# Kernel tuning notes

Measured on AMD Instinct MI355X. Metric: run time of the kernel, lower is better.

Reference implementation:

```python
import jax, jax.numpy as jnp
import numpy as np

NA, NP_, E = 40000, 60000, 80000
D, H = 512, 8
DK = D // H
SQRT_DK = float(DK) ** 0.5


def setup_inputs() -> dict:
    key = jax.random.key(0)
    ks = list(jax.random.split(key, 20))
    it = iter(ks)

    def nrm(shape, scale=1.0):
        return jax.random.normal(next(it), shape, dtype=jnp.float32) * scale

    xav = (6.0 / (DK + DK)) ** 0.5  # xavier_uniform bound for (dk, dk)
    w_scale = D ** -0.5
    inp = {
        "h_author": nrm((NA, D)),
        "h_paper": nrm((NP_, D)),
        "writes_src": jax.random.randint(next(it), (E,), 0, NA, dtype=jnp.int32),
        "writes_dst": jax.random.randint(next(it), (E,), 0, NP_, dtype=jnp.int32),
        "cites_src": jax.random.randint(next(it), (E,), 0, NP_, dtype=jnp.int32),
        "cites_dst": jax.random.randint(next(it), (E,), 0, NP_, dtype=jnp.int32),
        "wb_src": jax.random.randint(next(it), (E,), 0, NP_, dtype=jnp.int32),
        "wb_dst": jax.random.randint(next(it), (E,), 0, NA, dtype=jnp.int32),
        # per-node-type linear weights (2 types: 0=author, 1=paper)
        "Wk": nrm((2, D, D), w_scale), "bk": jnp.zeros((2, D), jnp.float32),
        "Wq": nrm((2, D, D), w_scale), "bq": jnp.zeros((2, D), jnp.float32),
        "Wv": nrm((2, D, D), w_scale), "bv": jnp.zeros((2, D), jnp.float32),
        "Wa": nrm((2, D, D), w_scale), "ba": jnp.zeros((2, D), jnp.float32),
        # per-relation params (3 relations: 0=writes, 1=cites, 2=written_by)
        "rel_att": jax.random.uniform(next(it), (3, H, DK, DK), jnp.float32, -xav, xav),
        "rel_msg": jax.random.uniform(next(it), (3, H, DK, DK), jnp.float32, -xav, xav),
        "rel_pri": jnp.ones((3, H), jnp.float32),
        "skip": jnp.ones((2,), jnp.float32),
    }
    return inp


def _edge_attn_agg(k, q, v, src, dst, pri, n_dst):
    # k, v: (N_src, H, DK) relation-transformed; q: (N_dst, H, DK)
    s = jnp.einsum('ehd,ehd->eh', q[dst], k[src]) * pri / SQRT_DK  # (E, H)
    m = jax.ops.segment_max(s, dst, num_segments=n_dst)            # edge softmax by dst
    ex = jnp.exp(s - m[dst])
    den = jax.ops.segment_sum(ex, dst, num_segments=n_dst)
    a = ex / den[dst]
    return jax.ops.segment_sum(v[src] * a[:, :, None], dst, num_segments=n_dst)


def reference(h_author, h_paper, writes_src, writes_dst, cites_src, cites_dst,
              wb_src, wb_dst, Wk, bk, Wq, bq, Wv, bv, Wa, ba,
              rel_att, rel_msg, rel_pri, skip):
    def proj(h, W, b, t):
        return (h @ W[t] + b[t]).reshape(-1, H, DK)

    k_a, v_a, q_a = proj(h_author, Wk, bk, 0), proj(h_author, Wv, bv, 0), proj(h_author, Wq, bq, 0)
    k_p, v_p, q_p = proj(h_paper, Wk, bk, 1), proj(h_paper, Wv, bv, 1), proj(h_paper, Wq, bq, 1)

    def rel(k, v, r):
        return (jnp.einsum('nhd,hde->nhe', k, rel_att[r]),
                jnp.einsum('nhd,hde->nhe', v, rel_msg[r]))

    k0, v0 = rel(k_a, v_a, 0)  # writes: author -> paper
    agg_w = _edge_attn_agg(k0, q_p, v0, writes_src, writes_dst, rel_pri[0], NP_)
    k1, v1 = rel(k_p, v_p, 1)  # cites: paper -> paper
    agg_c = _edge_attn_agg(k1, q_p, v1, cites_src, cites_dst, rel_pri[1], NP_)
    k2, v2 = rel(k_p, v_p, 2)  # written_by: paper -> author
    agg_b = _edge_attn_agg(k2, q_a, v2, wb_src, wb_dst, rel_pri[2], NA)

    t_paper = ((agg_w + agg_c) * 0.5).reshape(NP_, D)  # cross_reducer='mean'
    t_author = agg_b.reshape(NA, D)

    alpha = jax.nn.sigmoid(skip)
    out_a = (t_author @ Wa[0] + ba[0]) * alpha[0] + h_author * (1.0 - alpha[0])
    out_p = (t_paper @ Wa[1] + ba[1]) * alpha[1] + h_paper * (1.0 - alpha[1])
    return out_a, out_p
```

## Files before the change

### kernel.cpp

```cpp
#include <hip/hip_runtime.h>
#include <math.h>

#define D_ 512
#define H_ 8

typedef short bf16x8 __attribute__((ext_vector_type(8)));
typedef float f32x4 __attribute__((ext_vector_type(4)));

struct Outs { void* p[5]; };

__device__ __forceinline__ unsigned short f2bf(float x) {
  unsigned int u = __float_as_uint(x);
  unsigned int r = (u + 0x7fff + ((u >> 16) & 1)) >> 16;
  return (unsigned short)r;
}
__device__ __forceinline__ float bf2f(unsigned short b) {
  return __uint_as_float(((unsigned int)b) << 16);
}

__global__ void fill_kernel(float* __restrict__ p, float v, long n) {
  long i = (long)blockIdx.x * blockDim.x + threadIdx.x;
  long st = (long)gridDim.x * blockDim.x;
  for (; i < n; i += st) p[i] = v;
}

__global__ void convert_bf16_kernel(const float* __restrict__ in,
                                    unsigned short* __restrict__ out, long n8) {
  long i = (long)blockIdx.x * blockDim.x + threadIdx.x;
  long st = (long)gridDim.x * blockDim.x;
  for (; i < n8; i += st) {
    float4 a = ((const float4*)in)[i * 2];
    float4 b = ((const float4*)in)[i * 2 + 1];
    bf16x8 o;
    o[0] = (short)f2bf(a.x); o[1] = (short)f2bf(a.y);
    o[2] = (short)f2bf(a.z); o[3] = (short)f2bf(a.w);
    o[4] = (short)f2bf(b.x); o[5] = (short)f2bf(b.y);
    o[6] = (short)f2bf(b.z); o[7] = (short)f2bf(b.w);
    ((bf16x8*)out)[i] = o;
  }
}

__global__ void transpose_bf16_kernel(const float* __restrict__ W,
                                      unsigned short* __restrict__ Wt) {
  int n = blockIdx.x;
  int k = threadIdx.x;
  Wt[(long)n * D_ + k] = f2bf(W[(long)k * D_ + n]);
}

__global__ void copy_bias_kernel(const float* __restrict__ in,
                                 float* __restrict__ out) {
  out[threadIdx.x] = in[threadIdx.x];
}

__global__ void fuse_weight_kernel(const float* __restrict__ Win,
                                   const float* __restrict__ bin,
                                   const float* __restrict__ rel,
                                   unsigned short* __restrict__ Wf,
                                   float* __restrict__ bf) {
  int row = blockIdx.x;
  int j = threadIdx.x;
  int h = j >> 6, e = j & 63;
  const float* src = (row < D_) ? (Win + (long)row * D_) : bin;
  const float* rl = rel + h * 64 * 64;
  float acc = 0.f;
#pragma unroll 16
  for (int d = 0; d < 64; ++d) acc = fmaf(src[h * 64 + d], rl[d * 64 + e], acc);
  if (row < D_) Wf[(long)j * D_ + row] = f2bf(acc);
  else bf[j] = acc;
}

__global__ void hist_kernel(const int* __restrict__ w_dst,
                            const int* __restrict__ c_dst,
                            const int* __restrict__ b_dst,
                            int* __restrict__ degree, int E, int NP) {
  int i = blockIdx.x * blockDim.x + threadIdx.x;
  if (i >= 3 * E) return;
  int r = i / E, e = i - r * E;
  int d, base;
  if (r == 0)      { d = w_dst[e]; base = 0; }
  else if (r == 1) { d = c_dst[e]; base = NP; }
  else             { d = b_dst[e]; base = 2 * NP; }
  atomicAdd(degree + base + d, 1);
}

__global__ void scan1_kernel(const int* __restrict__ in, int* __restrict__ out,
                             int* __restrict__ aux, int n) {
  __shared__ int tmp[256];
  int t = threadIdx.x;
  int i = blockIdx.x * 256 + t;
  int v = (i < n) ? in[i] : 0;
  tmp[t] = v;
  __syncthreads();
#pragma unroll
  for (int d = 1; d < 256; d <<= 1) {
    int add = (t >= d) ? tmp[t - d] : 0;
    __syncthreads();
    tmp[t] += add;
    __syncthreads();
  }
  if (i < n) out[i] = tmp[t] - v;
  if (t == 255) aux[blockIdx.x] = tmp[255];
}

__global__ void scan2_kernel(int* __restrict__ aux, int nb) {
  __shared__ int tmp[1024];
  int t = threadIdx.x;
  int v = (t < nb) ? aux[t] : 0;
  tmp[t] = v;
  __syncthreads();
#pragma unroll
  for (int d = 1; d < 1024; d <<= 1) {
    int add = (t >= d) ? tmp[t - d] : 0;
    __syncthreads();
    tmp[t] += add;
    __syncthreads();
  }
  if (t < nb) aux[t] = tmp[t] - v;
}

__global__ void scan3_kernel(int* __restrict__ starts, int* __restrict__ cursor,
                             const int* __restrict__ aux, int n) {
  int i = blockIdx.x * 256 + threadIdx.x;
  if (i >= n) return;
  int s = starts[i] + aux[blockIdx.x];
  starts[i] = s;
  cursor[i] = s;
}

__global__ void scatter_kernel(const int* __restrict__ w_src, const int* __restrict__ w_dst,
                               const int* __restrict__ c_src, const int* __restrict__ c_dst,
                               const int* __restrict__ b_src, const int* __restrict__ b_dst,
                               int* __restrict__ cursor, int* __restrict__ csr,
                               int E, int NP) {
  int i = blockIdx.x * blockDim.x + threadIdx.x;
  if (i >= 3 * E) return;
  int r = i / E, e = i - r * E;
  int s, d, base;
  if (r == 0)      { s = w_src[e]; d = w_dst[e]; base = 0; }
  else if (r == 1) { s = c_src[e]; d = c_dst[e]; base = NP; }
  else             { s = b_src[e]; d = b_dst[e]; base = 2 * NP; }
  int pos = atomicAdd(cursor + base + d, 1);
  csr[pos] = s;
}

template <int TWO_LISTS>
__global__ __launch_bounds__(256) void attn_kernel(
    const unsigned short* __restrict__ q,
    const unsigned short* __restrict__ k0, const unsigned short* __restrict__ v0,
    const unsigned short* __restrict__ k1, const unsigned short* __restrict__ v1,
    const int* __restrict__ csr, const int* __restrict__ starts,
    const int* __restrict__ degree, int base0, int base1,
    const float* __restrict__ pri, int poff0, int poff1,
    unsigned short* __restrict__ out, int n_nodes, float outscale) {
  int gw = (int)(((long)blockIdx.x * blockDim.x + threadIdx.x) >> 6);
  if (gw >= n_nodes) return;
  int lane = threadIdx.x & 63;
  int h = lane >> 3, off = (lane & 7) << 3;
  const long rowoff = (long)gw * D_ + h * 64 + off;
  bf16x8 qv = *(const bf16x8*)(q + rowoff);
  float qf[8];
#pragma unroll
  for (int r = 0; r < 8; ++r) qf[r] = bf2f((unsigned short)qv[r]);

  float res[8] = {};

  auto process = [&](const unsigned short* K, const unsigned short* V,
                     int base, float ps) {
    int st = starts[base + gw], dg = degree[base + gw];
    float m = -INFINITY, l = 0.f;
    float acc[8] = {};
    for (int i = 0; i < dg; ++i) {
      int s = csr[st + i];
      const long ro = (long)s * D_ + h * 64 + off;
      bf16x8 kv = *(const bf16x8*)(K + ro);
      bf16x8 vv = *(const bf16x8*)(V + ro);
      float dot = 0.f;
#pragma unroll
      for (int r = 0; r < 8; ++r)
        dot = fmaf(qf[r], bf2f((unsigned short)kv[r]), dot);
      dot += __shfl_xor(dot, 1);
      dot += __shfl_xor(dot, 2);
      dot += __shfl_xor(dot, 4);
      float sc = dot * ps;
      float mn = fmaxf(m, sc);
      float scale = __expf(m - mn);
      float p = __expf(sc - mn);
      l = l * scale + p;
#pragma unroll
      for (int r = 0; r < 8; ++r)
        acc[r] = acc[r] * scale + p * bf2f((unsigned short)vv[r]);
      m = mn;
    }
    if (l > 0.f) {
      float inv = 1.f / l;
#pragma unroll
      for (int r = 0; r < 8; ++r) res[r] += acc[r] * inv;
    }
  };

  process(k0, v0, base0, pri[poff0 + h] * 0.125f);
  if (TWO_LISTS) process(k1, v1, base1, pri[poff1 + h] * 0.125f);

  bf16x8 o;
#pragma unroll
  for (int r = 0; r < 8; ++r) o[r] = (short)f2bf(res[r] * outscale);
  *(bf16x8*)(out + rowoff) = o;
}

__device__ __forceinline__ void gload_lds16(const void* g, void* l) {
  __builtin_amdgcn_global_load_lds(
      (const __attribute__((address_space(1))) void*)g,
      (__attribute__((address_space(3))) void*)l, 16, 0, 0);
}

template <int OUT_BF16, int WITH_SKIP>
__global__ __launch_bounds__(256) void gemm_mfma(
    const unsigned short* __restrict__ A,
    const unsigned short* __restrict__ Bt,
    const float* __restrict__ bias,
    Outs outs, int M, int GX, float a_scale,
    const float* __restrict__ Hres,
    const float* __restrict__ skip, int skip_idx) {
  __shared__ unsigned short Asm[128 * 64];
  __shared__ unsigned short Bsm[128 * 64];

  const int nwg = gridDim.x;
  const int orig = blockIdx.x;
  const int q8 = nwg >> 3, r8 = nwg & 7;
  const int xcd = orig & 7, pos = orig >> 3;
  const int wgid =
      (xcd < r8 ? xcd * (q8 + 1) : r8 * (q8 + 1) + (xcd - r8) * q8) + pos;
  const int bm = (wgid / GX) * 128;
  const int bn = (wgid % GX) * 128;

  const int tid = threadIdx.x;
  const int wave = tid >> 6, lane = tid & 63;
  const int wm = (wave >> 1) * 64, wn = (wave & 1) * 64;
  const int srow = tid >> 3;
  const int swz = ((tid & 7) ^ (srow & 7)) * 8;

  f32x4 acc[4][4] = {};

  const int rr = lane & 15;
  const int rx = (rr & 7) << 4;

  for (int k0 = 0; k0 < D_; k0 += 64) {
#pragma unroll
    for (int i = 0; i < 4; ++i) {
      int gr = bm + srow + i * 32;
      if (gr >= M) gr = M - 1;
      gload_lds16(A + (long)gr * D_ + k0 + swz, Asm + i * 2048 + wave * 512);
    }
#pragma unroll
    for (int i = 0; i < 4; ++i) {
      int gr = bn + srow + i * 32;
      gload_lds16(Bt + (long)gr * D_ + k0 + swz, Bsm + i * 2048 + wave * 512);
    }
    __syncthreads();
#pragma unroll
    for (int kk = 0; kk < 2; ++kk) {
      const int cb = kk * 64 + (lane >> 4) * 16;
      const int cs = cb ^ rx;
      bf16x8 af[4], bfr[4];
#pragma unroll
      for (int i = 0; i < 4; ++i)
        af[i] = *(const bf16x8*)((const char*)Asm + (wm + i * 16 + rr) * 128 + cs);
#pragma unroll
      for (int j = 0; j < 4; ++j)
        bfr[j] = *(const bf16x8*)((const char*)Bsm + (wn + j * 16 + rr) * 128 + cs);
#pragma unroll
      for (int i = 0; i < 4; ++i)
#pragma unroll
        for (int j = 0; j < 4; ++j)
          acc[i][j] = __builtin_amdgcn_mfma_f32_16x16x32_bf16(
              af[i], bfr[j], acc[i][j], 0, 0, 0);
    }
    __syncthreads();
  }

  float alpha = 1.f, beta = 0.f;
  if (WITH_SKIP) {
    float sv = skip[skip_idx];
    alpha = 1.f / (1.f + expf(-sv));
    beta = 1.f - alpha;
  }
  const int cr = (lane >> 4) * 4;
  const int cc = lane & 15;
  const int matu = (bn + wn) >> 9;
  const int wcb = (bn + wn) & 511;
  unsigned short* ob16 = (unsigned short*)outs.p[matu];
  float* ob32 = (float*)outs.p[0];
#pragma unroll
  for (int i = 0; i < 4; ++i) {
    int rowb = bm + wm + i * 16 + cr;
#pragma unroll
    for (int j = 0; j < 4; ++j) {
      int col = bn + wn + j * 16 + cc;
      float bb = bias[col];
#pragma unroll
      for (int r = 0; r < 4; ++r) {
        int row = rowb + r;
        if (row >= M) continue;
        float val = acc[i][j][r] * a_scale + bb;
        if (WITH_SKIP) val = val * alpha + Hres[(long)row * D_ + col] * beta;
        if (OUT_BF16)
          ob16[(long)row * D_ + wcb + j * 16 + cc] = f2bf(val);
        else
          ob32[(long)row * D_ + col] = val;
      }
    }
  }
}

extern "C" void kernel_launch(void* const* d_in, const int* in_sizes, int n_in,
                              void* d_out, int out_size, void* d_ws, size_t ws_size,
                              hipStream_t stream) {
  const float* h_author = (const float*)d_in[0];
  const float* h_paper  = (const float*)d_in[1];
  const int* w_src = (const int*)d_in[2];
  const int* w_dst = (const int*)d_in[3];
  const int* c_src = (const int*)d_in[4];
  const int* c_dst = (const int*)d_in[5];
  const int* b_src = (const int*)d_in[6];
  const int* b_dst = (const int*)d_in[7];
  const float* Wk = (const float*)d_in[8];
  const float* bk = (const float*)d_in[9];
  const float* Wq = (const float*)d_in[10];
  const float* bq = (const float*)d_in[11];
  const float* Wv = (const float*)d_in[12];
  const float* bv = (const float*)d_in[13];
  const float* Wa = (const float*)d_in[14];
  const float* ba = (const float*)d_in[15];
  const float* rel_att = (const float*)d_in[16];
  const float* rel_msg = (const float*)d_in[17];
  const float* rel_pri = (const float*)d_in[18];
  const float* skip = (const float*)d_in[19];

  const int NA = in_sizes[0] / D_;
  const int NP = in_sizes[1] / D_;
  const int E  = in_sizes[2];
  const long nmax = (NA > NP) ? NA : NP;
  const int NT = 2 * NP + NA;

  char* w = (char*)d_ws;
  auto alloc = [&](long bytes) {
    char* p = w;
    w += (bytes + 255) & ~255L;
    return p;
  };
  unsigned short* hA16 = (unsigned short*)alloc((long)NA * D_ * 2);
  unsigned short* hP16 = (unsigned short*)alloc((long)NP * D_ * 2);
  unsigned short* Pq   = (unsigned short*)alloc((long)NP * D_ * 2);
  unsigned short* Pkc  = (unsigned short*)alloc((long)NP * D_ * 2);
  unsigned short* Pvc  = (unsigned short*)alloc((long)NP * D_ * 2);
  unsigned short* Pkb  = (unsigned short*)alloc((long)NP * D_ * 2);
  unsigned short* Pvb  = (unsigned short*)alloc((long)NP * D_ * 2);
  unsigned short* Aq   = (unsigned short*)alloc((long)NA * D_ * 2);
  unsigned short* Akw  = (unsigned short*)alloc((long)NA * D_ * 2);
  unsigned short* Avw  = (unsigned short*)alloc((long)NA * D_ * 2);
  unsigned short* t16  = (unsigned short*)alloc(nmax * D_ * 2);
  unsigned short* BtP  = (unsigned short*)alloc((long)2560 * D_ * 2);
  unsigned short* BtA  = (unsigned short*)alloc((long)1536 * D_ * 2);
  float* bfP           = (float*)alloc(2560 * 4);
  float* bfA           = (float*)alloc(1536 * 4);
  unsigned short* Wa0t = (unsigned short*)alloc((long)D_ * D_ * 2);
  unsigned short* Wa1t = (unsigned short*)alloc((long)D_ * D_ * 2);
  int* degree          = (int*)alloc((long)NT * 4);
  int* starts          = (int*)alloc((long)NT * 4);
  int* cursor          = (int*)alloc((long)NT * 4);
  int* csr             = (int*)alloc((long)3 * E * 4);
  int* aux             = (int*)alloc(((long)NT / 256 + 2) * 4);

  const long WD = (long)D_ * D_;
  const long RS = (long)H_ * 64 * 64;
  const long SEG = (long)D_ * D_;

  auto fill = [&](float* p, float v, long n) {
    long b = (n + 255) / 256;
    int blocks = (int)(b > 4096 ? 4096 : b);
    fill_kernel<<<blocks, 256, 0, stream>>>(p, v, n);
  };
  auto cvt = [&](const float* in, unsigned short* out, long n) {
    long n8 = n / 8;
    long b = (n8 + 255) / 256;
    int blocks = (int)(b > 2048 ? 2048 : b);
    convert_bf16_kernel<<<blocks, 256, 0, stream>>>(in, out, n8);
  };

  float* out_a = (float*)d_out;
  float* out_p = out_a + (long)NA * D_;

  cvt(h_author, hA16, (long)NA * D_);
  cvt(h_paper, hP16, (long)NP * D_);

  fill((float*)degree, 0.f, NT);
  {
    int th = 3 * E;
    hist_kernel<<<(th + 255) / 256, 256, 0, stream>>>(w_dst, c_dst, b_dst,
                                                      degree, E, NP);
    int nb = (NT + 255) / 256;
    scan1_kernel<<<nb, 256, 0, stream>>>(degree, starts, aux, NT);
    scan2_kernel<<<1, 1024, 0, stream>>>(aux, nb);
    scan3_kernel<<<nb, 256, 0, stream>>>(starts, cursor, aux, NT);
    scatter_kernel<<<(th + 255) / 256, 256, 0, stream>>>(
        w_src, w_dst, c_src, c_dst, b_src, b_dst, cursor, csr, E, NP);
  }

  transpose_bf16_kernel<<<D_, D_, 0, stream>>>(Wq + WD, BtP);
  copy_bias_kernel<<<1, D_, 0, stream>>>(bq + D_, bfP);
  fuse_weight_kernel<<<513, 512, 0, stream>>>(Wk + WD, bk + D_, rel_att + RS,
                                              BtP + SEG, bfP + 512);
  fuse_weight_kernel<<<513, 512, 0, stream>>>(Wv + WD, bv + D_, rel_msg + RS,
                                              BtP + 2 * SEG, bfP + 1024);
  fuse_weight_kernel<<<513, 512, 0, stream>>>(Wk + WD, bk + D_, rel_att + 2 * RS,
                                              BtP + 3 * SEG, bfP + 1536);
  fuse_weight_kernel<<<513, 512, 0, stream>>>(Wv + WD, bv + D_, rel_msg + 2 * RS,
                                              BtP + 4 * SEG, bfP + 2048);

  transpose_bf16_kernel<<<D_, D_, 0, stream>>>(Wq, BtA);
  copy_bias_kernel<<<1, D_, 0, stream>>>(bq, bfA);
  fuse_weight_kernel<<<513, 512, 0, stream>>>(Wk, bk, rel_att,
                                              BtA + SEG, bfA + 512);
  fuse_weight_kernel<<<513, 512, 0, stream>>>(Wv, bv, rel_msg,
                                              BtA + 2 * SEG, bfA + 1024);

  transpose_bf16_kernel<<<D_, D_, 0, stream>>>(Wa, Wa0t);
  transpose_bf16_kernel<<<D_, D_, 0, stream>>>(Wa + WD, Wa1t);

  {
    Outs o; o.p[0] = Pq; o.p[1] = Pkc; o.p[2] = Pvc; o.p[3] = Pkb; o.p[4] = Pvb;
    int gy = (NP + 127) / 128;
    gemm_mfma<1, 0><<<20 * gy, 256, 0, stream>>>(
        hP16, BtP, bfP, o, NP, 20, 1.f, nullptr, nullptr, 0);
  }
  {
    Outs o; o.p[0] = Aq; o.p[1] = Akw; o.p[2] = Avw; o.p[3] = Aq; o.p[4] = Aq;
    int gy = (NA + 127) / 128;
    gemm_mfma<1, 0><<<12 * gy, 256, 0, stream>>>(
        hA16, BtA, bfA, o, NA, 12, 1.f, nullptr, nullptr, 0);
  }

  {
    long th = (long)NP * 64;
    attn_kernel<1><<<(int)((th + 255) / 256), 256, 0, stream>>>(
        Pq, Akw, Avw, Pkc, Pvc, csr, starts, degree, 0, NP,
        rel_pri, 0, H_, t16, NP, 0.5f);
  }
  {
    Outs o; o.p[0] = out_p; o.p[1] = o.p[2] = o.p[3] = o.p[4] = out_p;
    int gy = (NP + 127) / 128;
    gemm_mfma<0, 1><<<4 * gy, 256, 0, stream>>>(
        t16, Wa1t, ba + D_, o, NP, 4, 1.f, h_paper, skip, 1);
  }

  {
    long th = (long)NA * 64;
    attn_kernel<0><<<(int)((th + 255) / 256), 256, 0, stream>>>(
        Aq, Pkb, Pvb, Pkb, Pvb, csr, starts, degree, 2 * NP, 2 * NP,
        rel_pri, 2 * H_, 2 * H_, t16, NA, 1.f);
  }
  {
    Outs o; o.p[0] = out_a; o.p[1] = o.p[2] = o.p[3] = o.p[4] = out_a;
    int gy = (NA + 127) / 128;
    gemm_mfma<0, 1><<<4 * gy, 256, 0, stream>>>(
        t16, Wa0t, ba, o, NA, 4, 1.f, h_author, skip, 0);
  }
}
```

Baseline: 1.064 ms.

## Enlarge GEMM tiles to 256x256 with double-buffered async LDS prefetch

Rewrites the MFMA GEMM to use 256x256 output tiles with 512 threads, each wave computing a 128x64 subtile. The K loop is double-buffered: global-to-LDS loads for the next stages are issued ahead, with explicit vmcnt waits and raw barriers, and MFMA issue priority is raised. This aims to hide global load latency and raise data reuse per LDS byte, in exchange for 128KB of LDS per block, more accumulator registers, fewer blocks per GEMM (worse tail and occupancy), and a hand-tuned waitcnt scheme that must match the load count per stage.

```diff
diff --git a/kernel.cpp b/kernel.cpp
--- a/kernel.cpp
+++ b/kernel.cpp
@@ -214,15 +214,15 @@
 }
 
 template <int OUT_BF16, int WITH_SKIP>
-__global__ __launch_bounds__(256) void gemm_mfma(
+__global__ __launch_bounds__(512, 2) void gemm_mfma(
     const unsigned short* __restrict__ A,
     const unsigned short* __restrict__ Bt,
     const float* __restrict__ bias,
     Outs outs, int M, int GX, float a_scale,
     const float* __restrict__ Hres,
     const float* __restrict__ skip, int skip_idx) {
-  __shared__ unsigned short Asm[128 * 64];
-  __shared__ unsigned short Bsm[128 * 64];
+  __shared__ unsigned short Asm[2][256 * 64];
+  __shared__ unsigned short Bsm[2][256 * 64];
 
   const int nwg = gridDim.x;
   const int orig = blockIdx.x;
@@ -230,52 +230,74 @@
   const int xcd = orig & 7, pos = orig >> 3;
   const int wgid =
       (xcd < r8 ? xcd * (q8 + 1) : r8 * (q8 + 1) + (xcd - r8) * q8) + pos;
-  const int bm = (wgid / GX) * 128;
-  const int bn = (wgid % GX) * 128;
+  const int bm = (wgid / GX) * 256;
+  const int bn = (wgid % GX) * 256;
 
   const int tid = threadIdx.x;
   const int wave = tid >> 6, lane = tid & 63;
-  const int wm = (wave >> 1) * 64, wn = (wave & 1) * 64;
+  const int wm = (wave >> 2) * 128;
+  const int wn = (wave & 3) * 64;
   const int srow = tid >> 3;
   const int swz = ((tid & 7) ^ (srow & 7)) * 8;
 
-  f32x4 acc[4][4] = {};
+  f32x4 acc[8][4] = {};
 
   const int rr = lane & 15;
   const int rx = (rr & 7) << 4;
 
-  for (int k0 = 0; k0 < D_; k0 += 64) {
+  auto STAGE = [&](int buf, int kt) {
+    const int k0 = kt * 64;
 #pragma unroll
     for (int i = 0; i < 4; ++i) {
-      int gr = bm + srow + i * 32;
+      int gr = bm + srow + i * 64;
       if (gr >= M) gr = M - 1;
-      gload_lds16(A + (long)gr * D_ + k0 + swz, Asm + i * 2048 + wave * 512);
+      gload_lds16(A + (long)gr * D_ + k0 + swz, &Asm[buf][i * 4096 + wave * 512]);
     }
 #pragma unroll
     for (int i = 0; i < 4; ++i) {
-      int gr = bn + srow + i * 32;
-      gload_lds16(Bt + (long)gr * D_ + k0 + swz, Bsm + i * 2048 + wave * 512);
-    }
-    __syncthreads();
+      int gr = bn + srow + i * 64;
+      gload_lds16(Bt + (long)gr * D_ + k0 + swz, &Bsm[buf][i * 4096 + wave * 512]);
+    }
+  };
+
+  STAGE(0, 0);
+  STAGE(1, 1);
+
+#pragma unroll
+  for (int t = 0; t < 8; ++t) {
+    const int p = t & 1;
+    if (t == 7) asm volatile("s_waitcnt vmcnt(0)" ::: "memory");
+    else        asm volatile("s_waitcnt vmcnt(8)" ::: "memory");
+    __builtin_amdgcn_s_barrier();
+    asm volatile("" ::: "memory");
+
 #pragma unroll
     for (int kk = 0; kk < 2; ++kk) {
       const int cb = kk * 64 + (lane >> 4) * 16;
       const int cs = cb ^ rx;
-      bf16x8 af[4], bfr[4];
-#pragma unroll
-      for (int i = 0; i < 4; ++i)
-        af[i] = *(const bf16x8*)((const char*)Asm + (wm + i * 16 + rr) * 128 + cs);
-#pragma unroll
-      for (int j = 0; j < 4; ++j)
-        bfr[j] = *(const bf16x8*)((const char*)Bsm + (wn + j * 16 + rr) * 128 + cs);
-#pragma unroll
-      for (int i = 0; i < 4; ++i)
-#pragma unroll
-        for (int j = 0; j < 4; ++j)
-          acc[i][j] = __builtin_amdgcn_mfma_f32_16x16x32_bf16(
-              af[i], bfr[j], acc[i][j], 0, 0, 0);
-    }
-    __syncthreads();
+      bf16x8 af[8], bfr[4];
+#pragma unroll
+      for (int mi = 0; mi < 8; ++mi)
+        af[mi] = *(const bf16x8*)((const char*)&Asm[p][0] +
+                                  (wm + mi * 16 + rr) * 128 + cs);
+#pragma unroll
+      for (int nj = 0; nj < 4; ++nj)
+        bfr[nj] = *(const bf16x8*)((const char*)&Bsm[p][0] +
+                                   (wn + nj * 16 + rr) * 128 + cs);
+      __builtin_amdgcn_s_setprio(1);
+#pragma unroll
+      for (int mi = 0; mi < 8; ++mi)
+#pragma unroll
+        for (int nj = 0; nj < 4; ++nj)
+          acc[mi][nj] = __builtin_amdgcn_mfma_f32_16x16x32_bf16(
+              af[mi], bfr[nj], acc[mi][nj], 0, 0, 0);
+      __builtin_amdgcn_s_setprio(0);
+    }
+
+    asm volatile("" ::: "memory");
+    __builtin_amdgcn_s_barrier();
+    asm volatile("" ::: "memory");
+    if (t + 2 < 8) STAGE(p, t + 2);
   }
 
   float alpha = 1.f, beta = 0.f;
@@ -291,20 +313,20 @@
   unsigned short* ob16 = (unsigned short*)outs.p[matu];
   float* ob32 = (float*)outs.p[0];
 #pragma unroll
-  for (int i = 0; i < 4; ++i) {
-    int rowb = bm + wm + i * 16 + cr;
-#pragma unroll
-    for (int j = 0; j < 4; ++j) {
-      int col = bn + wn + j * 16 + cc;
+  for (int mi = 0; mi < 8; ++mi) {
+    int rowb = bm + wm + mi * 16 + cr;
+#pragma unroll
+    for (int nj = 0; nj < 4; ++nj) {
+      int col = bn + wn + nj * 16 + cc;
       float bb = bias[col];
 #pragma unroll
       for (int r = 0; r < 4; ++r) {
         int row = rowb + r;
         if (row >= M) continue;
-        float val = acc[i][j][r] * a_scale + bb;
+        float val = acc[mi][nj][r] * a_scale + bb;
         if (WITH_SKIP) val = val * alpha + Hres[(long)row * D_ + col] * beta;
         if (OUT_BF16)
-          ob16[(long)row * D_ + wcb + j * 16 + cc] = f2bf(val);
+          ob16[(long)row * D_ + wcb + nj * 16 + cc] = f2bf(val);
         else
           ob32[(long)row * D_ + col] = val;
       }
@@ -429,15 +451,15 @@
 
   {
     Outs o; o.p[0] = Pq; o.p[1] = Pkc; o.p[2] = Pvc; o.p[3] = Pkb; o.p[4] = Pvb;
-    int gy = (NP + 127) / 128;
-    gemm_mfma<1, 0><<<20 * gy, 256, 0, stream>>>(
-        hP16, BtP, bfP, o, NP, 20, 1.f, nullptr, nullptr, 0);
+    int gy = (NP + 255) / 256;
+    gemm_mfma<1, 0><<<10 * gy, 512, 0, stream>>>(
+        hP16, BtP, bfP, o, NP, 10, 1.f, nullptr, nullptr, 0);
   }
   {
     Outs o; o.p[0] = Aq; o.p[1] = Akw; o.p[2] = Avw; o.p[3] = Aq; o.p[4] = Aq;
-    int gy = (NA + 127) / 128;
-    gemm_mfma<1, 0><<<12 * gy, 256, 0, stream>>>(
-        hA16, BtA, bfA, o, NA, 12, 1.f, nullptr, nullptr, 0);
+    int gy = (NA + 255) / 256;
+    gemm_mfma<1, 0><<<6 * gy, 512, 0, stream>>>(
+        hA16, BtA, bfA, o, NA, 6, 1.f, nullptr, nullptr, 0);
   }
 
   {
@@ -448,9 +470,9 @@
   }
   {
     Outs o; o.p[0] = out_p; o.p[1] = o.p[2] = o.p[3] = o.p[4] = out_p;
-    int gy = (NP + 127) / 128;
-    gemm_mfma<0, 1><<<4 * gy, 256, 0, stream>>>(
-        t16, Wa1t, ba + D_, o, NP, 4, 1.f, h_paper, skip, 1);
+    int gy = (NP + 255) / 256;
+    gemm_mfma<0, 1><<<2 * gy, 512, 0, stream>>>(
+        t16, Wa1t, ba + D_, o, NP, 2, 1.f, h_paper, skip, 1);
   }
 
   {
@@ -461,8 +483,8 @@
   }
   {
     Outs o; o.p[0] = out_a; o.p[1] = o.p[2] = o.p[3] = o.p[4] = out_a;
-    int gy = (NA + 127) / 128;
-    gemm_mfma<0, 1><<<4 * gy, 256, 0, stream>>>(
-        t16, Wa0t, ba, o, NA, 4, 1.f, h_author, skip, 0);
-  }
-}
+    int gy = (NA + 255) / 256;
+    gemm_mfma<0, 1><<<2 * gy, 512, 0, stream>>>(
+        t16, Wa0t, ba, o, NA, 2, 1.f, h_author, skip, 0);
+  }
+}
```

Result: faster. 985.5 us (-7.4%).
